# Optimization experiments

Hardware: AMD Instinct MI355X
Metric: run time of the kernel (lower is better)

Reference implementation:

```python
import jax, jax.numpy as jnp
import numpy as np

# ---- problem sizes ----
N_NEURONS = 1536
N_INPUTS = 768
BATCH = 32
T = 256
DT = 1.0  # ms per step
SURRGRAD_SCALE = 10.0

# ---- per-cell-type physiology (recurrent): 0=excitatory, 1=inhibitory ----
CELL_TAU_MEM = np.array([20.0, 10.0], np.float32)   # ms
CELL_THETA   = np.array([-50.0, -50.0], np.float32) # mV
CELL_URESET  = np.array([-65.0, -65.0], np.float32) # mV
CELL_EL      = np.array([-65.0, -65.0], np.float32) # mV
CELL_GL      = np.array([10.0, 10.0], np.float32)   # nS
CELL_TAUREF  = np.array([2.0, 1.0], np.float32)     # ms

# ---- synapse types: AMPA(pre=exc), NMDA(pre=exc), GABA_A(pre=inh) ----
SYN_CELL_ID   = np.array([0, 0, 1], np.int32)
SYN_TAU_RISE  = np.array([0.5, 2.0, 0.5], np.float32)
SYN_TAU_DECAY = np.array([2.0, 100.0, 5.0], np.float32)
SYN_EREV      = np.array([0.0, 0.0, -70.0], np.float32)
SYN_GBAR      = np.array([1.0, 0.5, 1.0], np.float32)

# ---- feedforward: single excitatory input type, single AMPA synapse ----
FF_TAU_RISE, FF_TAU_DECAY, FF_EREV, FF_GBAR = 0.5, 2.0, 0.0, 1.0


@jax.custom_vjp
def spike(v):
    # Heaviside spike with fast-sigmoid surrogate gradient
    return (v >= 0).astype(v.dtype)

def _spike_fwd(v):
    return spike(v), v

def _spike_bwd(v, g):
    return (g / (SURRGRAD_SCALE * jnp.abs(v) + 1.0) ** 2,)

spike.defvjp(_spike_fwd, _spike_bwd)


def setup_inputs() -> dict:
    key = jax.random.key(0)
    ks = jax.random.split(key, 6)
    input_spikes = (jax.random.uniform(ks[0], (BATCH, T, N_INPUTS)) < 0.05).astype(jnp.float32)
    weights = jax.random.normal(ks[1], (N_NEURONS, N_NEURONS), jnp.float32) * 0.05
    weights_FF = jax.random.normal(ks[2], (N_INPUTS, N_NEURONS), jnp.float32) * 0.05
    cell_type_indices = jax.random.randint(ks[3], (N_NEURONS,), 0, 2, jnp.int32)
    cell_type_indices_FF = jnp.zeros((N_INPUTS,), jnp.int32)
    scaling_factors = jax.random.uniform(ks[4], (2, 2), jnp.float32, 0.5, 1.5)
    scaling_factors_FF = jax.random.uniform(ks[5], (1, 2), jnp.float32, 0.5, 1.5)
    return {
        'input_spikes': input_spikes,
        'weights': weights,
        'weights_FF': weights_FF,
        'scaling_factors': scaling_factors,
        'scaling_factors_FF': scaling_factors_FF,
        'cell_type_indices': cell_type_indices,
        'cell_type_indices_FF': cell_type_indices_FF,
    }


def _simulate(input_spikes, weights, weights_FF, scaling_factors, scaling_factors_FF,
              cell_type_indices, cell_type_indices_FF):
    ct = cell_type_indices
    B = input_spikes.shape[0]

    # per-neuron physiology gathered by cell type
    tau_mem = jnp.asarray(CELL_TAU_MEM)[ct]
    theta = jnp.asarray(CELL_THETA)[ct]
    u_reset = jnp.asarray(CELL_URESET)[ct]
    e_l = jnp.asarray(CELL_EL)[ct]
    g_l = jnp.asarray(CELL_GL)[ct]
    ref_steps = jnp.asarray(CELL_TAUREF)[ct] / DT
    leak_coef = DT / (tau_mem * g_l)  # dt / C_m

    # effective weights: cell-type scaling + presynaptic synapse-type mask
    sf = scaling_factors[ct[:, None], ct[None, :]]            # (N, N)
    W = weights * sf
    pre_mask = (jnp.asarray(SYN_CELL_ID)[:, None] == ct[None, :]).astype(W.dtype)  # (S, N)
    Ws = W[None, :, :] * pre_mask[:, :, None]                  # (S, N, N)
    sfF = scaling_factors_FF[cell_type_indices_FF[:, None], ct[None, :]]
    WF = weights_FF * sfF                                      # (n_in, N)

    alpha_r = jnp.exp(-DT / jnp.asarray(SYN_TAU_RISE))[:, None, None]   # (S,1,1)
    alpha_d = jnp.exp(-DT / jnp.asarray(SYN_TAU_DECAY))[:, None, None]
    arF = jnp.exp(jnp.float32(-DT / FF_TAU_RISE))
    adF = jnp.exp(jnp.float32(-DT / FF_TAU_DECAY))
    gbar = jnp.asarray(SYN_GBAR)
    gbarE = jnp.asarray(SYN_GBAR * SYN_EREV)
    S = gbar.shape[0]

    U0 = jnp.broadcast_to(e_l, (B, N_NEURONS))
    carry0 = (U0,
              jnp.zeros((B, N_NEURONS), jnp.float32),       # previous spikes
              jnp.zeros((S, B, N_NEURONS), jnp.float32),    # x (rise)
              jnp.zeros((S, B, N_NEURONS), jnp.float32),    # g (decay)
              jnp.zeros((B, N_NEURONS), jnp.float32),       # x_FF
              jnp.zeros((B, N_NEURONS), jnp.float32),       # g_FF
              jnp.zeros((B, N_NEURONS), jnp.float32))       # refractory counter

    def step(carry, I_t):
        U, s_prev, x, g, xF, gF, ref = carry
        # dual-exponential conductance update per synapse type
        inp = jnp.einsum('bn,snm->sbm', s_prev, Ws)
        x = alpha_r * x + inp
        g = alpha_d * g + x
        xF = arF * xF + I_t @ WF
        gF = adF * gF + xF
        # conductance-based synaptic current: sum_s gbar_s * g_s * (E_s - U)
        gtot = jnp.einsum('s,sbn->bn', gbar, g) + FF_GBAR * gF
        gE = jnp.einsum('s,sbn->bn', gbarE, g) + (FF_GBAR * FF_EREV) * gF
        I_syn = gE - gtot * U
        # leaky membrane integration
        U_new = U + leak_coef * (g_l * (e_l - U) + I_syn)
        # refractory clamp
        in_ref = ref > 0
        U_new = jnp.where(in_ref, u_reset, U_new)
        ref = jnp.maximum(ref - 1.0, 0.0)
        # surrogate-gradient spike and reset
        s_new = spike(U_new - theta)
        U_out = jnp.where(s_new > 0, u_reset, U_new)
        ref = jnp.where(s_new > 0, ref_steps, ref)
        return (U_out, s_new, x, g, xF, gF, ref), (s_new, U_out)

    I_seq = jnp.transpose(input_spikes, (1, 0, 2))  # (T, B, n_in)
    _, (spk, volts) = jax.lax.scan(step, carry0, I_seq)
    return jnp.transpose(spk, (1, 0, 2)), jnp.transpose(volts, (1, 0, 2))


def reference(input_spikes, weights, weights_FF, scaling_factors, scaling_factors_FF,
              cell_type_indices, cell_type_indices_FF):
    return _simulate(input_spikes, weights, weights_FF, scaling_factors, scaling_factors_FF,
                     cell_type_indices, cell_type_indices_FF)
```

## Files before the change

kernel.cpp:

```cpp
#include <hip/hip_runtime.h>
#include <stdint.h>


__global__ __launch_bounds__(768) void snn_lif_kernel(
    const float* __restrict__ I,
    const float* __restrict__ W,
    const float* __restrict__ WF,
    const float* __restrict__ sf,
    const float* __restrict__ sfF,
    const int*   __restrict__ ct,
    float* __restrict__ out,
    uint64_t* __restrict__ recpub)
{
    const int tid = threadIdx.x;
    const int j   = blockIdx.x & 7;
    const int b   = blockIdx.x >> 3;
    const int wv  = tid >> 6;
    const int wl  = tid & 63;

    __shared__ float4   part0[2][12][48];
    __shared__ float4   part1[2][12][48];
    __shared__ float4   partF[2][12][48];
    __shared__ uint32_t ctm32_sh[48];

    for (int r = 0; r < 2; ++r) {
        int c = ct[r * 768 + tid];
        uint64_t bal = __ballot(c != 0);
        if (wl == 0) {
            ctm32_sh[r * 24 + wv * 2]     = (uint32_t)bal;
            ctm32_sh[r * 24 + wv * 2 + 1] = (uint32_t)(bal >> 32);
        }
    }
    __syncthreads();

    const int m = j * 192 + ((tid < 192) ? tid : 0);
    const int   myct = ct[m];
    const float s0m  = sf[myct];
    const float s1m  = sf[2 + myct];
    const float sFm  = sfF[myct];
    const float lc   = (myct == 0) ? (1.0f / 200.0f) : (1.0f / 100.0f);
    const float refsteps = (myct == 0) ? 2.0f : 1.0f;
    const float ar0 = expf(-1.0f / 0.5f),  ad0 = expf(-1.0f / 2.0f);
    const float ar1 = expf(-1.0f / 2.0f),  ad1 = expf(-1.0f / 100.0f);
    const float ar2 = expf(-1.0f / 0.5f),  ad2 = expf(-1.0f / 5.0f);
    const float arF = expf(-1.0f / 0.5f),  adF = expf(-1.0f / 2.0f);

    float U = -65.0f, refc = 0.0f;
    float x0 = 0, g0 = 0, x1 = 0, g1 = 0, x2 = 0, g2 = 0, xF = 0, gF = 0;

    const int  btbase  = b * 256;
    const bool gl      = (wl < 48);
    const uint32_t colbase = (uint32_t)(j * 192 + wl * 4);

    uint64_t fmask;
    {
        float iv = __builtin_nontemporal_load(
            &I[(uint32_t)btbase * 768u + (uint32_t)tid]);
        fmask = __ballot(iv > 0.5f);
    }

    for (int t = 0; t < 256; ++t) {
        float ivn = 0.0f;
        if (t < 255)
            ivn = __builtin_nontemporal_load(
                &I[(uint32_t)(btbase + t + 1) * 768u + (uint32_t)tid]);

        float4 a0 = make_float4(0.f, 0.f, 0.f, 0.f);
        float4 a1 = a0, aF = a0;

        {
            uint64_t mm = fmask;
            while (mm) {
                const int bit = __builtin_ctzll(mm);
                mm &= mm - 1;
                const uint32_t row = (uint32_t)(wv * 64 + bit);
                if (gl) {
                    const float4 w = *(const float4*)(WF + row * 1536u + colbase);
                    aF.x += w.x; aF.y += w.y; aF.z += w.z; aF.w += w.w;
                }
            }
        }

        if (t > 0) {
            uint32_t ready = 0;
            const uint32_t pbase = (uint32_t)(btbase + t - 1) * 48u + (uint32_t)(wv * 4);
            do {
                uint64_t pv = 0;
                if (wl < 4)
                    pv = __hip_atomic_load(&recpub[pbase + (uint32_t)wl],
                                           __ATOMIC_RELAXED, __HIP_MEMORY_SCOPE_AGENT);
                const uint32_t plo = (uint32_t)pv;
                const uint32_t phi = (uint32_t)(pv >> 32);
                #pragma unroll
                for (int k = 0; k < 4; ++k) {
                    if (ready & (1u << k)) continue;
                    const uint32_t tg = __builtin_amdgcn_readlane(phi, k);
                    if (tg != (uint32_t)t) continue;
                    ready |= 1u << k;
                    uint32_t bits = __builtin_amdgcn_readlane(plo, k);
                    const uint32_t word = (uint32_t)(wv * 4 + k);
                    const uint32_t cm = ctm32_sh[word];
                    while (bits) {
                        const int bit = __builtin_ctz(bits);
                        bits &= bits - 1;
                        const uint32_t row = word * 32u + (uint32_t)bit;
                        if (gl) {
                            const float4 w = *(const float4*)(W + row * 1536u + colbase);
                            if ((cm >> bit) & 1u) {
                                a1.x += w.x; a1.y += w.y; a1.z += w.z; a1.w += w.w;
                            } else {
                                a0.x += w.x; a0.y += w.y; a0.z += w.z; a0.w += w.w;
                            }
                        }
                    }
                }
            } while (ready != 0xFu);
        }

        const int buf = t & 1;
        if (gl) {
            part0[buf][wv][wl] = a0;
            part1[buf][wv][wl] = a1;
            partF[buf][wv][wl] = aF;
        }
        fmask = __ballot(ivn > 0.5f);
        __syncthreads();

        if (tid < 192) {
            const float* p0 = (const float*)&part0[buf][0][0];
            const float* p1 = (const float*)&part1[buf][0][0];
            const float* pF = (const float*)&partF[buf][0][0];
            float z0s = 0.f, z1s = 0.f, zFs = 0.f;
            #pragma unroll
            for (int k = 0; k < 12; ++k) {
                z0s += p0[k * 192 + tid];
                z1s += p1[k * 192 + tid];
                zFs += pF[k * 192 + tid];
            }
            z0s *= s0m; z1s *= s1m; zFs *= sFm;
            x0 = ar0 * x0 + z0s;  g0 = ad0 * g0 + x0;
            x1 = ar1 * x1 + z0s;  g1 = ad1 * g1 + x1;
            x2 = ar2 * x2 + z1s;  g2 = ad2 * g2 + x2;
            xF = arF * xF + zFs;  gF = adF * gF + xF;
            const float gtot = g0 + 0.5f * g1 + g2 + gF;
            const float gE   = -70.0f * g2;
            const float Isyn = gE - gtot * U;
            float Un = U + lc * (10.0f * (-65.0f - U) + Isyn);
            if (refc > 0.0f) Un = -65.0f;
            refc = fmaxf(refc - 1.0f, 0.0f);
            const bool s = (Un - (-50.0f)) >= 0.0f;
            const uint64_t bal = __ballot(s);
            if (wl == 0 || wl == 32) {
                const uint32_t half = (wl == 0) ? (uint32_t)bal : (uint32_t)(bal >> 32);
                const uint32_t word = (uint32_t)(j * 6 + wv * 2) + (wl == 32 ? 1u : 0u);
                const uint32_t widx = (uint32_t)(btbase + t) * 48u + word;
                const uint64_t v = ((uint64_t)(uint32_t)(t + 1) << 32) | half;
                __hip_atomic_store(&recpub[widx], v, __ATOMIC_RELAXED,
                                   __HIP_MEMORY_SCOPE_AGENT);
            }
            const float Uo = s ? -65.0f : Un;
            refc = s ? refsteps : refc;
            U = Uo;
            const uint32_t oidx = (uint32_t)(btbase + t) * 1536u + (uint32_t)m;
            __builtin_nontemporal_store(s ? 1.0f : 0.0f, &out[oidx]);
            __builtin_nontemporal_store(Uo, &out[12582912u + oidx]);
        }
    }
}

extern "C" void kernel_launch(void* const* d_in, const int* in_sizes, int n_in,
                              void* d_out, int out_size, void* d_ws, size_t ws_size,
                              hipStream_t stream) {
    const float* I   = (const float*)d_in[0];
    const float* W   = (const float*)d_in[1];
    const float* WF  = (const float*)d_in[2];
    const float* sf  = (const float*)d_in[3];
    const float* sfF = (const float*)d_in[4];
    const int*   ct  = (const int*)d_in[5];

    uint64_t* recpub = (uint64_t*)d_ws;

    snn_lif_kernel<<<dim3(256), dim3(768), 0, stream>>>(
        I, W, WF, sf, sfF, ct, (float*)d_out, recpub);
}
```

Baseline: 748.1 us.

## Split each batch's neurons across 16 blocks instead of 8

Each block now owns 96 neurons instead of 192, and the launch grows from 256 to 512 persistent blocks. The goal is to halve the weight-gather and reduction work per block at every timestep and use more CUs. Each spike word is now split across blocks, so the publish logic is reworked to match. The per-word cell-type masks are hoisted into registers, and the lane guard on loads is dropped by clamping the column index. The cost is that only 24 of 64 lanes per wave do useful gathers. It also relies on all 512 spin-waiting blocks being resident at once, otherwise the kernel can deadlock.

Measured after the change: 884.9 us. 18.3% more time.

```diff
diff --git a/kernel.cpp b/kernel.cpp
--- a/kernel.cpp
+++ b/kernel.cpp
@@ -1,6 +1,8 @@
 #include <hip/hip_runtime.h>
 #include <stdint.h>
 
+
+#define ATOMIC_LD(p) __hip_atomic_load((p), __ATOMIC_RELAXED, __HIP_MEMORY_SCOPE_AGENT)
 
 __global__ __launch_bounds__(768) void snn_lif_kernel(
     const float* __restrict__ I,
@@ -13,14 +15,14 @@
     uint64_t* __restrict__ recpub)
 {
     const int tid = threadIdx.x;
-    const int j   = blockIdx.x & 7;
-    const int b   = blockIdx.x >> 3;
+    const int j   = blockIdx.x & 15;
+    const int b   = blockIdx.x >> 4;
     const int wv  = tid >> 6;
     const int wl  = tid & 63;
 
-    __shared__ float4   part0[2][12][48];
-    __shared__ float4   part1[2][12][48];
-    __shared__ float4   partF[2][12][48];
+    __shared__ float4   part0[2][12][24];
+    __shared__ float4   part1[2][12][24];
+    __shared__ float4   partF[2][12][24];
     __shared__ uint32_t ctm32_sh[48];
 
     for (int r = 0; r < 2; ++r) {
@@ -33,7 +35,11 @@
     }
     __syncthreads();
 
-    const int m = j * 192 + ((tid < 192) ? tid : 0);
+    uint32_t cmw[4];
+    #pragma unroll
+    for (int k = 0; k < 4; ++k) cmw[k] = ctm32_sh[wv * 4 + k];
+
+    const int m = j * 96 + ((tid < 96) ? tid : 0);
     const int   myct = ct[m];
     const float s0m  = sf[myct];
     const float s1m  = sf[2 + myct];
@@ -48,9 +54,9 @@
     float U = -65.0f, refc = 0.0f;
     float x0 = 0, g0 = 0, x1 = 0, g1 = 0, x2 = 0, g2 = 0, xF = 0, gF = 0;
 
-    const int  btbase  = b * 256;
-    const bool gl      = (wl < 48);
-    const uint32_t colbase = (uint32_t)(j * 192 + wl * 4);
+    const int  btbase = b * 256;
+    const bool gl     = (wl < 24);
+    const uint32_t colbase = (uint32_t)(j * 96) + (uint32_t)((wl < 24 ? wl : 23) * 4);
 
     uint64_t fmask;
     {
@@ -74,10 +80,8 @@
                 const int bit = __builtin_ctzll(mm);
                 mm &= mm - 1;
                 const uint32_t row = (uint32_t)(wv * 64 + bit);
-                if (gl) {
-                    const float4 w = *(const float4*)(WF + row * 1536u + colbase);
-                    aF.x += w.x; aF.y += w.y; aF.z += w.z; aF.w += w.w;
-                }
+                const float4 w = *(const float4*)(WF + (size_t)row * 1536u + colbase);
+                aF.x += w.x; aF.y += w.y; aF.z += w.z; aF.w += w.w;
             }
         }
 
@@ -87,30 +91,27 @@
             do {
                 uint64_t pv = 0;
                 if (wl < 4)
-                    pv = __hip_atomic_load(&recpub[pbase + (uint32_t)wl],
-                                           __ATOMIC_RELAXED, __HIP_MEMORY_SCOPE_AGENT);
+                    pv = ATOMIC_LD(&recpub[pbase + (uint32_t)wl]);
                 const uint32_t plo = (uint32_t)pv;
                 const uint32_t phi = (uint32_t)(pv >> 32);
                 #pragma unroll
                 for (int k = 0; k < 4; ++k) {
                     if (ready & (1u << k)) continue;
-                    const uint32_t tg = __builtin_amdgcn_readlane(phi, k);
+                    const uint32_t tg = (uint32_t)__builtin_amdgcn_readlane(phi, k);
                     if (tg != (uint32_t)t) continue;
                     ready |= 1u << k;
-                    uint32_t bits = __builtin_amdgcn_readlane(plo, k);
+                    uint32_t bits = (uint32_t)__builtin_amdgcn_readlane(plo, k);
+                    const uint32_t cm   = cmw[k];
                     const uint32_t word = (uint32_t)(wv * 4 + k);
-                    const uint32_t cm = ctm32_sh[word];
                     while (bits) {
                         const int bit = __builtin_ctz(bits);
                         bits &= bits - 1;
                         const uint32_t row = word * 32u + (uint32_t)bit;
-                        if (gl) {
-                            const float4 w = *(const float4*)(W + row * 1536u + colbase);
-                            if ((cm >> bit) & 1u) {
-                                a1.x += w.x; a1.y += w.y; a1.z += w.z; a1.w += w.w;
-                            } else {
-                                a0.x += w.x; a0.y += w.y; a0.z += w.z; a0.w += w.w;
-                            }
+                        const float4 w = *(const float4*)(W + (size_t)row * 1536u + colbase);
+                        if ((cm >> bit) & 1u) {
+                            a1.x += w.x; a1.y += w.y; a1.z += w.z; a1.w += w.w;
+                        } else {
+                            a0.x += w.x; a0.y += w.y; a0.z += w.z; a0.w += w.w;
                         }
                     }
                 }
@@ -126,16 +127,16 @@
         fmask = __ballot(ivn > 0.5f);
         __syncthreads();
 
-        if (tid < 192) {
+        if (tid < 96) {
             const float* p0 = (const float*)&part0[buf][0][0];
             const float* p1 = (const float*)&part1[buf][0][0];
             const float* pF = (const float*)&partF[buf][0][0];
             float z0s = 0.f, z1s = 0.f, zFs = 0.f;
             #pragma unroll
             for (int k = 0; k < 12; ++k) {
-                z0s += p0[k * 192 + tid];
-                z1s += p1[k * 192 + tid];
-                zFs += pF[k * 192 + tid];
+                z0s += p0[k * 96 + tid];
+                z1s += p1[k * 96 + tid];
+                zFs += pF[k * 96 + tid];
             }
             z0s *= s0m; z1s *= s1m; zFs *= sFm;
             x0 = ar0 * x0 + z0s;  g0 = ad0 * g0 + x0;
@@ -150,11 +151,17 @@
             refc = fmaxf(refc - 1.0f, 0.0f);
             const bool s = (Un - (-50.0f)) >= 0.0f;
             const uint64_t bal = __ballot(s);
-            if (wl == 0 || wl == 32) {
+            if (wv == 0 && (wl == 0 || wl == 32)) {
                 const uint32_t half = (wl == 0) ? (uint32_t)bal : (uint32_t)(bal >> 32);
-                const uint32_t word = (uint32_t)(j * 6 + wv * 2) + (wl == 32 ? 1u : 0u);
+                const uint32_t word = (uint32_t)(j * 3) + (wl == 32 ? 1u : 0u);
                 const uint32_t widx = (uint32_t)(btbase + t) * 48u + word;
                 const uint64_t v = ((uint64_t)(uint32_t)(t + 1) << 32) | half;
+                __hip_atomic_store(&recpub[widx], v, __ATOMIC_RELAXED,
+                                   __HIP_MEMORY_SCOPE_AGENT);
+            }
+            if (wv == 1 && wl == 0) {
+                const uint32_t widx = (uint32_t)(btbase + t) * 48u + (uint32_t)(j * 3 + 2);
+                const uint64_t v = ((uint64_t)(uint32_t)(t + 1) << 32) | (uint32_t)bal;
                 __hip_atomic_store(&recpub[widx], v, __ATOMIC_RELAXED,
                                    __HIP_MEMORY_SCOPE_AGENT);
             }
@@ -180,6 +187,6 @@
 
     uint64_t* recpub = (uint64_t*)d_ws;
 
-    snn_lif_kernel<<<dim3(256), dim3(768), 0, stream>>>(
+    snn_lif_kernel<<<dim3(512), dim3(768), 0, stream>>>(
         I, W, WF, sf, sfF, ct, (float*)d_out, recpub);
 }
```

## Add dedicated poller wave forwarding recurrent spike words via LDS mailbox

Applied to the files above, without the earlier changes.

Adds a 13th wavefront per block that alone polls the global recurrent-spike publication buffer and copies fresh words into an LDS mailbox. The 12 compute waves now spin on LDS instead of issuing agent-scope global atomic loads, and a shared done counter tells the poller when to stop. Each block also writes its own spike words straight into the mailbox. The aim is to cut polling latency and global memory traffic on the cross-block critical path, at the cost of one extra wave per block and more LDS synchronisation.

Result: slower. 782.7 us (+4.6%).

```diff
diff --git a/kernel.cpp b/kernel.cpp
--- a/kernel.cpp
+++ b/kernel.cpp
@@ -2,7 +2,13 @@
 #include <stdint.h>
 
 
-__global__ __launch_bounds__(768) void snn_lif_kernel(
+#define ATOMIC_LD(p)   __hip_atomic_load((p), __ATOMIC_RELAXED, __HIP_MEMORY_SCOPE_AGENT)
+#define LDS_LD32(p)    __hip_atomic_load((p), __ATOMIC_RELAXED, __HIP_MEMORY_SCOPE_WORKGROUP)
+#define LDS_ST32(p, v) __hip_atomic_store((p), (v), __ATOMIC_RELAXED, __HIP_MEMORY_SCOPE_WORKGROUP)
+#define LDS_LD64(p)    __hip_atomic_load((p), __ATOMIC_RELAXED, __HIP_MEMORY_SCOPE_WORKGROUP)
+#define LDS_ST64(p, v) __hip_atomic_store((p), (v), __ATOMIC_RELAXED, __HIP_MEMORY_SCOPE_WORKGROUP)
+
+__global__ __launch_bounds__(832) void snn_lif_kernel(
     const float* __restrict__ I,
     const float* __restrict__ W,
     const float* __restrict__ WF,
@@ -22,16 +28,29 @@
     __shared__ float4   part1[2][12][48];
     __shared__ float4   partF[2][12][48];
     __shared__ uint32_t ctm32_sh[48];
+    __shared__ uint64_t mb_sh[48];
+    __shared__ int      dc_sh[2];
+
+    if (tid < 48) mb_sh[tid] = 0;
+    if (tid == 0) { dc_sh[0] = 0; dc_sh[1] = 0; }
 
     for (int r = 0; r < 2; ++r) {
-        int c = ct[r * 768 + tid];
-        uint64_t bal = __ballot(c != 0);
-        if (wl == 0) {
-            ctm32_sh[r * 24 + wv * 2]     = (uint32_t)bal;
-            ctm32_sh[r * 24 + wv * 2 + 1] = (uint32_t)(bal >> 32);
+        if (tid < 768) {
+            int c = ct[r * 768 + tid];
+            uint64_t bal = __ballot(c != 0);
+            if (wl == 0) {
+                ctm32_sh[r * 24 + wv * 2]     = (uint32_t)bal;
+                ctm32_sh[r * 24 + wv * 2 + 1] = (uint32_t)(bal >> 32);
+            }
         }
     }
     __syncthreads();
+
+    uint32_t cmw[4] = {0, 0, 0, 0};
+    if (wv < 12) {
+        #pragma unroll
+        for (int k = 0; k < 4; ++k) cmw[k] = ctm32_sh[wv * 4 + k];
+    }
 
     const int m = j * 192 + ((tid < 192) ? tid : 0);
     const int   myct = ct[m];
@@ -52,77 +71,94 @@
     const bool gl      = (wl < 48);
     const uint32_t colbase = (uint32_t)(j * 192 + wl * 4);
 
-    uint64_t fmask;
+    uint64_t fmask = 0;
     {
-        float iv = __builtin_nontemporal_load(
-            &I[(uint32_t)btbase * 768u + (uint32_t)tid]);
+        float iv = 0.0f;
+        if (tid < 768)
+            iv = __builtin_nontemporal_load(
+                &I[(uint32_t)btbase * 768u + (uint32_t)tid]);
         fmask = __ballot(iv > 0.5f);
     }
 
     for (int t = 0; t < 256; ++t) {
+        const int buf = t & 1;
+
         float ivn = 0.0f;
-        if (t < 255)
+        if (t < 255 && tid < 768)
             ivn = __builtin_nontemporal_load(
                 &I[(uint32_t)(btbase + t + 1) * 768u + (uint32_t)tid]);
 
-        float4 a0 = make_float4(0.f, 0.f, 0.f, 0.f);
-        float4 a1 = a0, aF = a0;
-
-        {
-            uint64_t mm = fmask;
-            while (mm) {
-                const int bit = __builtin_ctzll(mm);
-                mm &= mm - 1;
-                const uint32_t row = (uint32_t)(wv * 64 + bit);
-                if (gl) {
-                    const float4 w = *(const float4*)(WF + row * 1536u + colbase);
-                    aF.x += w.x; aF.y += w.y; aF.z += w.z; aF.w += w.w;
+        if (wv == 12) {
+            if (t > 0) {
+                const uint32_t pbase = (uint32_t)(btbase + t - 1) * 48u;
+                for (;;) {
+                    uint64_t pv = 0;
+                    if (wl < 48)
+                        pv = ATOMIC_LD(&recpub[pbase + (uint32_t)wl]);
+                    if (wl < 48 && (uint32_t)(pv >> 32) == (uint32_t)t)
+                        LDS_ST64(&mb_sh[wl], pv);
+                    if (LDS_LD32(&dc_sh[buf]) == 12) break;
                 }
             }
-        }
-
-        if (t > 0) {
-            uint32_t ready = 0;
-            const uint32_t pbase = (uint32_t)(btbase + t - 1) * 48u + (uint32_t)(wv * 4);
-            do {
-                uint64_t pv = 0;
-                if (wl < 4)
-                    pv = __hip_atomic_load(&recpub[pbase + (uint32_t)wl],
-                                           __ATOMIC_RELAXED, __HIP_MEMORY_SCOPE_AGENT);
-                const uint32_t plo = (uint32_t)pv;
-                const uint32_t phi = (uint32_t)(pv >> 32);
-                #pragma unroll
-                for (int k = 0; k < 4; ++k) {
-                    if (ready & (1u << k)) continue;
-                    const uint32_t tg = __builtin_amdgcn_readlane(phi, k);
-                    if (tg != (uint32_t)t) continue;
-                    ready |= 1u << k;
-                    uint32_t bits = __builtin_amdgcn_readlane(plo, k);
-                    const uint32_t word = (uint32_t)(wv * 4 + k);
-                    const uint32_t cm = ctm32_sh[word];
-                    while (bits) {
-                        const int bit = __builtin_ctz(bits);
-                        bits &= bits - 1;
-                        const uint32_t row = word * 32u + (uint32_t)bit;
-                        if (gl) {
-                            const float4 w = *(const float4*)(W + row * 1536u + colbase);
-                            if ((cm >> bit) & 1u) {
-                                a1.x += w.x; a1.y += w.y; a1.z += w.z; a1.w += w.w;
-                            } else {
-                                a0.x += w.x; a0.y += w.y; a0.z += w.z; a0.w += w.w;
+        } else {
+            float4 a0 = make_float4(0.f, 0.f, 0.f, 0.f);
+            float4 a1 = a0, aF = a0;
+
+            {
+                uint64_t mm = fmask;
+                while (mm) {
+                    const int bit = __builtin_ctzll(mm);
+                    mm &= mm - 1;
+                    const uint32_t row = (uint32_t)(wv * 64 + bit);
+                    if (gl) {
+                        const float4 w = *(const float4*)(WF + row * 1536u + colbase);
+                        aF.x += w.x; aF.y += w.y; aF.z += w.z; aF.w += w.w;
+                    }
+                }
+            }
+
+            if (t > 0) {
+                uint32_t ready = 0;
+                do {
+                    uint64_t pv = 0;
+                    if (wl < 4)
+                        pv = LDS_LD64(&mb_sh[wv * 4 + wl]);
+                    const uint32_t plo = (uint32_t)pv;
+                    const uint32_t phi = (uint32_t)(pv >> 32);
+                    #pragma unroll
+                    for (int k = 0; k < 4; ++k) {
+                        if (ready & (1u << k)) continue;
+                        const uint32_t tg = (uint32_t)__builtin_amdgcn_readlane(phi, k);
+                        if (tg != (uint32_t)t) continue;
+                        ready |= 1u << k;
+                        uint32_t bits = (uint32_t)__builtin_amdgcn_readlane(plo, k);
+                        const uint32_t cm   = cmw[k];
+                        const uint32_t word = (uint32_t)(wv * 4 + k);
+                        while (bits) {
+                            const int bit = __builtin_ctz(bits);
+                            bits &= bits - 1;
+                            const uint32_t row = word * 32u + (uint32_t)bit;
+                            if (gl) {
+                                const float4 w = *(const float4*)(W + row * 1536u + colbase);
+                                if ((cm >> bit) & 1u) {
+                                    a1.x += w.x; a1.y += w.y; a1.z += w.z; a1.w += w.w;
+                                } else {
+                                    a0.x += w.x; a0.y += w.y; a0.z += w.z; a0.w += w.w;
+                                }
                             }
                         }
                     }
-                }
-            } while (ready != 0xFu);
+                } while (ready != 0xFu);
+                if (wl == 0) atomicAdd(&dc_sh[buf], 1);
+            }
+
+            if (gl) {
+                part0[buf][wv][wl] = a0;
+                part1[buf][wv][wl] = a1;
+                partF[buf][wv][wl] = aF;
+            }
         }
 
-        const int buf = t & 1;
-        if (gl) {
-            part0[buf][wv][wl] = a0;
-            part1[buf][wv][wl] = a1;
-            partF[buf][wv][wl] = aF;
-        }
         fmask = __ballot(ivn > 0.5f);
         __syncthreads();
 
@@ -155,6 +191,7 @@
                 const uint32_t word = (uint32_t)(j * 6 + wv * 2) + (wl == 32 ? 1u : 0u);
                 const uint32_t widx = (uint32_t)(btbase + t) * 48u + word;
                 const uint64_t v = ((uint64_t)(uint32_t)(t + 1) << 32) | half;
+                LDS_ST64(&mb_sh[word], v);
                 __hip_atomic_store(&recpub[widx], v, __ATOMIC_RELAXED,
                                    __HIP_MEMORY_SCOPE_AGENT);
             }
@@ -165,6 +202,8 @@
             __builtin_nontemporal_store(s ? 1.0f : 0.0f, &out[oidx]);
             __builtin_nontemporal_store(Uo, &out[12582912u + oidx]);
         }
+
+        if (tid == 768) LDS_ST32(&dc_sh[buf], 0);
     }
 }
 
@@ -180,6 +219,6 @@
 
     uint64_t* recpub = (uint64_t*)d_ws;
 
-    snn_lif_kernel<<<dim3(256), dim3(768), 0, stream>>>(
+    snn_lif_kernel<<<dim3(256), dim3(832), 0, stream>>>(
         I, W, WF, sf, sfF, ct, (float*)d_out, recpub);
 }
```
